# Performance work log

Hardware: AMD Instinct MI355X
Metric: run time of the kernel (lower is better)

The kernel has to match this reference:

```python
import jax, jax.numpy as jnp
import numpy as np

B, NV, H, D = 8, 16, 192, 512
NH = 8
HD = D // NH
DFF = 2048
EPS = 1e-5


def _bn(x, g, b):
    # x: (N, T, C); BatchNorm1d over channel C using batch stats (train mode)
    mu = jnp.mean(x, axis=(0, 1))
    var = jnp.var(x, axis=(0, 1))
    return (x - mu) / jnp.sqrt(var + EPS) * g + b


def _ff(x, w1, b1, w2, b2):
    h = jax.nn.gelu(jnp.einsum('bnhd,fd->bnhf', x, w1) + b1, approximate=False)
    return jnp.einsum('bnhf,df->bnhd', h, w2) + b2


def setup_inputs() -> dict:
    key = jax.random.key(0)
    ks = jax.random.split(key, 20)
    s = 0.02
    return {
        'src': jax.random.normal(ks[0], (B, NV, H, D), jnp.float32),
        'qk_w': jax.random.normal(ks[1], (2 * D, D), jnp.float32) * s,
        'qk_b': jnp.zeros((2 * D,), jnp.float32),
        'v_w': jax.random.normal(ks[2], (D, D), jnp.float32) * s,
        'v_b': jnp.zeros((D,), jnp.float32),
        'alpha_p': jax.random.normal(ks[3], (HD, 1), jnp.float32) * 0.1,
        'g_pre1': jnp.ones((D,), jnp.float32),
        'b_pre1': jnp.zeros((D,), jnp.float32),
        'g_pre2': jnp.ones((D,), jnp.float32),
        'b_pre2': jnp.zeros((D,), jnp.float32),
        'ff1_w1': jax.random.normal(ks[4], (DFF, D), jnp.float32) * s,
        'ff1_b1': jnp.zeros((DFF,), jnp.float32),
        'ff1_w2': jax.random.normal(ks[5], (D, DFF), jnp.float32) * s,
        'ff1_b2': jnp.zeros((D,), jnp.float32),
        'ff2_w1': jax.random.normal(ks[6], (DFF, D), jnp.float32) * s,
        'ff2_b1': jnp.zeros((DFF,), jnp.float32),
        'ff2_w2': jax.random.normal(ks[7], (D, DFF), jnp.float32) * s,
        'ff2_b2': jnp.zeros((D,), jnp.float32),
        'g_attn': jnp.ones((D,), jnp.float32),
        'b_attn': jnp.zeros((D,), jnp.float32),
    }


def reference(src, qk_w, qk_b, v_w, v_b, alpha_p,
              g_pre1, b_pre1, g_pre2, b_pre2,
              ff1_w1, ff1_b1, ff1_w2, ff1_b2,
              ff2_w1, ff2_b1, ff2_w2, ff2_b2,
              g_attn, b_attn):
    b, n, h, c = src.shape
    hd = c // NH
    # normalized input for q,k; raw for v
    src1 = src / jnp.linalg.norm(src, axis=-1, keepdims=True)
    qk = (jnp.einsum('bnhc,ec->bnhe', src1, qk_w) + qk_b)
    qk = qk.reshape(b, n, h, 2, NH, hd).transpose(3, 0, 1, 4, 2, 5)  # (2,b,n,NH,h,hd)
    q, k = qk[0], qk[1]
    v = (jnp.einsum('bnhc,ec->bnhe', src, v_w) + v_b)
    v = v.reshape(b, n, h, NH, hd).transpose(0, 1, 3, 2, 4)  # (b,n,NH,h,hd)

    # exponential-decay weights in FFT domain (branch: h != 7)
    a = jax.nn.sigmoid(alpha_p)                  # (hd,1)
    ar = jnp.arange(h - 1, -1, -1, dtype=src.dtype)
    weights = a * (1.0 - a) ** ar                # (hd, h)
    n2 = 2 * h
    w_f = jnp.fft.rfft(weights, n=n2, axis=-1)   # (hd, h+1)
    q_f = jnp.swapaxes(jnp.fft.rfft(q, n=n2, axis=-2), -1, -2) * w_f
    k_f = jnp.swapaxes(jnp.fft.rfft(k, n=n2, axis=-2), -1, -2) * w_f
    q1 = jnp.swapaxes(jnp.fft.irfft(q_f, n=n2, axis=-1)[..., :h], -1, -2)
    k1 = jnp.swapaxes(jnp.fft.irfft(k_f, n=n2, axis=-1)[..., :h], -1, -2)

    # token-axis attention (note: original divides by head_dim**-0.5 == * sqrt(hd))
    score_t = jnp.einsum('bnhed,bnhfd->bnhef', q1, k1) * (hd ** 0.5)
    attn_t = jax.nn.softmax(score_t, axis=-1)
    out_tok = jnp.einsum('bnhef,bnhfd->bnhed', attn_t, v)  # (b,n,NH,h,hd)
    o3 = _bn(out_tok.reshape(b * n, h, NH * hd), g_pre2, b_pre2).reshape(b, n, h, c)

    # hidden-axis attention on un-decayed q,k (scale = sqrt(h))
    score_h = jnp.einsum('bnhae,bnhaf->bnhef', q, k) * (h ** 0.5)
    attn_h = jax.nn.softmax(score_h, axis=-1)
    out_hid = jnp.einsum('bnhef,bnhaf->bnhae', attn_h, v)  # (b,n,NH,h,hd)
    o2 = _bn(out_hid.reshape(b * n, h, NH * hd), g_pre1, b_pre1).reshape(b, n, h, c)

    src2 = _ff(o3, ff1_w1, ff1_b1, ff1_w2, ff1_b2) + _ff(o2, ff2_w1, ff2_b1, ff2_w2, ff2_b2)
    out = src + src2
    out = _bn(out.reshape(b * n, h, c), g_attn, b_attn).reshape(b, n, h, c)
    return out
```

## Files before the change

### kernel.cpp

```cpp
#include <hip/hip_runtime.h>
#include <math.h>

#define SEQ 192
#define NTOK 24576
#define EPS 1e-5f

typedef __bf16 bf16x8 __attribute__((ext_vector_type(8)));
typedef __bf16 bf16x4 __attribute__((ext_vector_type(4)));
typedef float  f32x4  __attribute__((ext_vector_type(4)));

__device__ __forceinline__ void load_lds16(const __bf16* g, __bf16* l) {
    __builtin_amdgcn_global_load_lds(
        (const __attribute__((address_space(1))) uint32_t*)g,
        (__attribute__((address_space(3))) uint32_t*)l, 16, 0, 0);
}

__device__ __forceinline__ float gelu_f(float x) {
    float z = 1.5957691216057308f * x * fmaf(0.044715f, x*x, 1.f);
    float e = __expf(-z);
    return x * __builtin_amdgcn_rcpf(1.f + e);
}

__global__ __launch_bounds__(256) void cvtall_k(
    const float* __restrict__ s0, const float* __restrict__ s1, const float* __restrict__ s2,
    const float* __restrict__ s3, const float* __restrict__ s4, const float* __restrict__ s5,
    __bf16* __restrict__ dst)
{
    int i = blockIdx.x * 256 + threadIdx.x;
    int f = i * 4;
    const float* s; int off;
    if      (f <  524288) { s = s0; off = 0;       }
    else if (f <  786432) { s = s1; off = 524288;  }
    else if (f < 1835008) { s = s2; off = 786432;  }
    else if (f < 2883584) { s = s3; off = 1835008; }
    else if (f < 3932160) { s = s4; off = 2883584; }
    else                  { s = s5; off = 3932160; }
    f32x4 v = *(const f32x4*)&s[f - off];
    bf16x4 o;
    o[0]=(__bf16)v[0]; o[1]=(__bf16)v[1]; o[2]=(__bf16)v[2]; o[3]=(__bf16)v[3];
    ((bf16x4*)dst)[i] = o;
}

__global__ __launch_bounds__(256) void prep_k(const float* __restrict__ src,
    __bf16* __restrict__ srcb, __bf16* __restrict__ srcnb)
{
    int w = threadIdx.x >> 6, lane = threadIdx.x & 63;
    size_t token = blockIdx.x * 4 + w;
    const float* p = src + token * 512 + lane * 8;
    f32x4 a0 = *(const f32x4*)p;
    f32x4 a1 = *(const f32x4*)(p + 4);
    float s = a0[0]*a0[0]+a0[1]*a0[1]+a0[2]*a0[2]+a0[3]*a0[3]
            + a1[0]*a1[0]+a1[1]*a1[1]+a1[2]*a1[2]+a1[3]*a1[3];
#pragma unroll
    for (int off = 32; off; off >>= 1) s += __shfl_xor(s, off);
    float rs = rsqrtf(s);
    bf16x8 vb, vn;
#pragma unroll
    for (int q = 0; q < 4; q++) {
        vb[q]   = (__bf16)a0[q];      vn[q]   = (__bf16)(a0[q]*rs);
        vb[q+4] = (__bf16)a1[q];      vn[q+4] = (__bf16)(a1[q]*rs);
    }
    *(bf16x8*)&srcb[token*512 + lane*8]  = vb;
    *(bf16x8*)&srcnb[token*512 + lane*8] = vn;
}

template<bool AFFINE, bool GELU>
__global__ __launch_bounds__(256) void gemm_k(
    const __bf16* __restrict__ A, const __bf16* __restrict__ B, __bf16* __restrict__ C,
    int N, int K, const float* __restrict__ bias, const float* __restrict__ coef)
{
    __shared__ __bf16 As[8192];
    __shared__ __bf16 Bs[8192];
    const int tid = threadIdx.x, lane = tid & 63, w = tid >> 6;
    const int wr = w >> 1, wc = w & 1;
    const int b = blockIdx.y * gridDim.x + blockIdx.x;
    const int xcd = b & 7, bi = b >> 3;
    const int ypx = gridDim.y >> 3;
    const int m0 = (xcd * ypx + bi / gridDim.x) * 128;
    const int n0 = (bi % gridDim.x) * 128;
    const int fr = lane & 15, fq = lane >> 4;
    const int grow = 8*w + (lane >> 3);
    const int gcol = ((lane & 7) ^ (lane >> 3)) * 8;
    const __bf16* gB = B + (size_t)(n0 + grow) * K + gcol;
    const __bf16* gA = A + (size_t)(m0 + grow) * K + gcol;
    __bf16* ldsA = As + 8*w*64 + lane*8;
    __bf16* ldsB = Bs + 8*w*64 + lane*8;

    f32x4 acc[4][4];
#pragma unroll
    for (int i = 0; i < 4; i++)
#pragma unroll
        for (int j = 0; j < 4; j++) acc[i][j] = (f32x4){0.f,0.f,0.f,0.f};

    for (int k0 = 0; k0 < K; k0 += 64) {
        if (!AFFINE) {
#pragma unroll
            for (int i = 0; i < 4; i++)
                load_lds16(gA + k0 + (size_t)(32*i)*K, ldsA + i*2048);
        } else {
            const int r = tid >> 3, cseg = tid & 7;
            const float* scp = coef + k0 + cseg*8;
            const float* shp = coef + 512 + k0 + cseg*8;
            f32x4 sc0 = *(const f32x4*)scp, sc1 = *(const f32x4*)(scp+4);
            f32x4 sh0 = *(const f32x4*)shp, sh1 = *(const f32x4*)(shp+4);
#pragma unroll
            for (int i = 0; i < 4; i++) {
                int row = 32*i + r;
                bf16x8 a = *(const bf16x8*)&A[(size_t)(m0+row)*512 + k0 + cseg*8];
                bf16x8 v;
#pragma unroll
                for (int q = 0; q < 4; q++) {
                    v[q]   = (__bf16)fmaf((float)a[q],   sc0[q], sh0[q]);
                    v[q+4] = (__bf16)fmaf((float)a[q+4], sc1[q], sh1[q]);
                }
                *(bf16x8*)&As[row*64 + ((cseg ^ (r & 7)) * 8)] = v;
            }
        }
#pragma unroll
        for (int i = 0; i < 4; i++)
            load_lds16(gB + k0 + (size_t)(32*i)*K, ldsB + i*2048);
        __syncthreads();
#pragma unroll
        for (int kk = 0; kk < 2; kk++) {
            bf16x8 af[4], bfv[4];
#pragma unroll
            for (int i = 0; i < 4; i++)
                af[i] = *(bf16x8*)&As[(wr*64 + i*16 + fr)*64 + (((kk*4+fq) ^ (fr&7))*8)];
#pragma unroll
            for (int j = 0; j < 4; j++)
                bfv[j] = *(bf16x8*)&Bs[(wc*64 + j*16 + fr)*64 + (((kk*4+fq) ^ (fr&7))*8)];
#pragma unroll
            for (int i = 0; i < 4; i++)
#pragma unroll
                for (int j = 0; j < 4; j++)
                    acc[i][j] = __builtin_amdgcn_mfma_f32_16x16x32_bf16(af[i], bfv[j], acc[i][j], 0, 0, 0);
        }
        __syncthreads();
    }
    const int r4 = lane >> 4, cc = lane & 15;
#pragma unroll
    for (int i = 0; i < 4; i++) {
#pragma unroll
        for (int r = 0; r < 4; r++) {
            int m = m0 + wr*64 + i*16 + r4*4 + r;
#pragma unroll
            for (int j = 0; j < 4; j++) {
                int n = n0 + wc*64 + j*16 + cc;
                float v = acc[i][j][r] + bias[n];
                if (GELU) v = gelu_f(v);
                C[(size_t)m * N + n] = (__bf16)v;
            }
        }
    }
}

__global__ __launch_bounds__(256) void gemm2_k(
    const __bf16* __restrict__ A1, const __bf16* __restrict__ A2,
    const __bf16* __restrict__ B1, const __bf16* __restrict__ B2,
    float* __restrict__ C, const float* __restrict__ b1, const float* __restrict__ b2,
    const float* __restrict__ resid, float* __restrict__ st)
{
    __shared__ __bf16 As[4096];
    __shared__ __bf16 Bs[8192];
    const int tid = threadIdx.x, lane = tid & 63, w = tid >> 6;
    const int wr = w >> 1, wc = w & 1;
    const int vb = blockIdx.x;
    const int xcd = vb & 7, k2 = vb >> 3;
    const int m0 = (xcd*24 + (k2 >> 2)) * 64;
    const int n0 = (k2 & 3) * 128;
    const int fr = lane & 15, fq = lane >> 4;
    const int grow = 8*w + (lane >> 3);
    const int gcol = ((lane & 7) ^ (lane >> 3)) * 8;
    const int K = 2048;
    __bf16* ldsA = As + 8*w*64 + lane*8;
    __bf16* ldsB = Bs + 8*w*64 + lane*8;

    f32x4 acc[2][4];
#pragma unroll
    for (int i = 0; i < 2; i++)
#pragma unroll
        for (int j = 0; j < 4; j++) acc[i][j] = (f32x4){0.f,0.f,0.f,0.f};

#pragma unroll 1
    for (int half = 0; half < 2; half++) {
        const __bf16* gA = (half ? A2 : A1) + (size_t)(m0 + grow) * K + gcol;
        const __bf16* gB = (half ? B2 : B1) + (size_t)(n0 + grow) * K + gcol;
        for (int k0 = 0; k0 < K; k0 += 64) {
            load_lds16(gA + k0,                 ldsA);
            load_lds16(gA + k0 + (size_t)32*K,  ldsA + 2048);
#pragma unroll
            for (int i = 0; i < 4; i++)
                load_lds16(gB + k0 + (size_t)(32*i)*K, ldsB + i*2048);
            __syncthreads();
#pragma unroll
            for (int kk = 0; kk < 2; kk++) {
                bf16x8 af[2], bfv[4];
#pragma unroll
                for (int i = 0; i < 2; i++)
                    af[i] = *(bf16x8*)&As[(wr*32 + i*16 + fr)*64 + (((kk*4+fq) ^ (fr&7))*8)];
#pragma unroll
                for (int j = 0; j < 4; j++)
                    bfv[j] = *(bf16x8*)&Bs[(wc*64 + j*16 + fr)*64 + (((kk*4+fq) ^ (fr&7))*8)];
#pragma unroll
                for (int i = 0; i < 2; i++)
#pragma unroll
                    for (int j = 0; j < 4; j++)
                        acc[i][j] = __builtin_amdgcn_mfma_f32_16x16x32_bf16(af[i], bfv[j], acc[i][j], 0, 0, 0);
            }
            __syncthreads();
        }
    }
    const int r4 = lane >> 4, cc = lane & 15;
    float cs[4] = {0,0,0,0}, cq[4] = {0,0,0,0};
#pragma unroll
    for (int i = 0; i < 2; i++) {
#pragma unroll
        for (int r = 0; r < 4; r++) {
            int m = m0 + wr*32 + i*16 + r4*4 + r;
#pragma unroll
            for (int j = 0; j < 4; j++) {
                int n = n0 + wc*64 + j*16 + cc;
                size_t idx = (size_t)m * 512 + n;
                float v = acc[i][j][r] + b1[n] + b2[n] + resid[idx];
                C[idx] = v;
                cs[j] += v; cq[j] = fmaf(v, v, cq[j]);
            }
        }
    }
#pragma unroll
    for (int j = 0; j < 4; j++) {
        cs[j] += __shfl_xor(cs[j], 16); cs[j] += __shfl_xor(cs[j], 32);
        cq[j] += __shfl_xor(cq[j], 16); cq[j] += __shfl_xor(cq[j], 32);
    }
    if (r4 == 0) {
#pragma unroll
        for (int j = 0; j < 4; j++) {
            int n = n0 + wc*64 + j*16 + cc;
            atomicAdd(&st[n], cs[j]);
            atomicAdd(&st[512 + n], cq[j]);
        }
    }
}

__global__ __launch_bounds__(256) void decay_scan_k(__bf16* __restrict__ QKb, const float* __restrict__ alpha)
{
    int g = blockIdx.x * 256 + threadIdx.x;
    int bn = g >> 8, e4 = (g & 255) * 4;
    int ai = e4 & 63;
    f32x4 a, rr;
#pragma unroll
    for (int j = 0; j < 4; j++) { float av = 1.f/(1.f + __expf(-alpha[ai + j])); a[j] = av; rr[j] = 1.f - av; }
    __bf16* p = QKb + (size_t)bn * SEQ * 1024 + e4;
    f32x4 P = {0,0,0,0}, pw = {1,1,1,1};
    for (int t = 0; t < SEQ; t++) {
        bf16x4 v = *(bf16x4*)&p[(size_t)t*1024];
        f32x4 vf = { (float)v[0], (float)v[1], (float)v[2], (float)v[3] };
        P += pw * vf;
        bf16x4 o;
#pragma unroll
        for (int j = 0; j < 4; j++) o[j] = (__bf16)P[j];
        *(bf16x4*)&p[(size_t)t*1024] = o;
        pw *= rr;
    }
    f32x4 f = a;
    for (int t = SEQ-1; t >= 0; t--) {
        bf16x4 v = *(bf16x4*)&p[(size_t)t*1024];
        bf16x4 o;
#pragma unroll
        for (int j = 0; j < 4; j++) o[j] = (__bf16)((float)v[j] * f[j]);
        *(bf16x4*)&p[(size_t)t*1024] = o;
        f *= rr;
    }
}

__global__ __launch_bounds__(256) void hidden_attn_mfma_k(
    const __bf16* __restrict__ QKb, const __bf16* __restrict__ Vb, __bf16* __restrict__ OHb)
{
    __shared__ __bf16 smem[25600];
    __bf16* Qt = smem;
    __bf16* Kt = smem + 12800;
    __bf16* Ps = smem;
    __bf16* Vs = smem + 4608;
    const int bn = blockIdx.x >> 3, nh = blockIdx.x & 7;
    const int tid = threadIdx.x, lane = tid & 63, w = tid >> 6;
    const int fr = lane & 15, fq = lane >> 4;
    const size_t rowbase = (size_t)bn * SEQ;

#pragma unroll
    for (int it = 0; it < 12; it++) {
        int tk = tid + (it % 6) * 256;
        int j = tk & 63, tg = tk >> 6;
        const __bf16* gsrc = QKb + (rowbase + tg*8)*1024 + nh*64 + j + (it >= 6 ? 512 : 0);
        bf16x8 v;
#pragma unroll
        for (int u = 0; u < 8; u++) v[u] = gsrc[(size_t)u*1024];
        __bf16* dst = (it >= 6 ? Kt : Qt) + j*200 + tg*8;
        *(bf16x8*)dst = v;
    }
    __syncthreads();

    f32x4 acc[4];
#pragma unroll
    for (int i = 0; i < 4; i++) acc[i] = (f32x4){0.f,0.f,0.f,0.f};
#pragma unroll
    for (int kc = 0; kc < 6; kc++) {
        bf16x8 a = *(bf16x8*)&Qt[(w*16 + fr)*200 + kc*32 + fq*8];
#pragma unroll
        for (int nt = 0; nt < 4; nt++) {
            bf16x8 b = *(bf16x8*)&Kt[(nt*16 + fr)*200 + kc*32 + fq*8];
            acc[nt] = __builtin_amdgcn_mfma_f32_16x16x32_bf16(a, b, acc[nt], 0, 0, 0);
        }
    }
    const float sc = 13.856406460551018f;
    float pn[4][4];
#pragma unroll
    for (int reg = 0; reg < 4; reg++) {
        float m = -1e30f;
#pragma unroll
        for (int nt = 0; nt < 4; nt++) { acc[nt][reg] *= sc; m = fmaxf(m, acc[nt][reg]); }
#pragma unroll
        for (int off = 1; off < 16; off <<= 1) m = fmaxf(m, __shfl_xor(m, off));
        float l = 0.f;
#pragma unroll
        for (int nt = 0; nt < 4; nt++) { pn[nt][reg] = __expf(acc[nt][reg] - m); l += pn[nt][reg]; }
#pragma unroll
        for (int off = 1; off < 16; off <<= 1) l += __shfl_xor(l, off);
        float inv = 1.f / l;
#pragma unroll
        for (int nt = 0; nt < 4; nt++) pn[nt][reg] *= inv;
    }
    __syncthreads();
#pragma unroll
    for (int nt = 0; nt < 4; nt++)
#pragma unroll
        for (int reg = 0; reg < 4; reg++)
            Ps[(w*16 + fq*4 + reg)*72 + nt*16 + fr] = (__bf16)pn[nt][reg];
    for (int i = tid; i < 1536; i += 256) {
        int t = i >> 3, s = i & 7;
        *(bf16x8*)&Vs[t*72 + s*8] = *(const bf16x8*)&Vb[(rowbase+t)*512 + nh*64 + s*8];
    }
    __syncthreads();

    f32x4 o[3][4];
#pragma unroll
    for (int i = 0; i < 3; i++)
#pragma unroll
        for (int j = 0; j < 4; j++) o[i][j] = (f32x4){0.f,0.f,0.f,0.f};
#pragma unroll
    for (int kc = 0; kc < 2; kc++) {
        bf16x8 av[3];
#pragma unroll
        for (int mt = 0; mt < 3; mt++)
            av[mt] = *(bf16x8*)&Vs[(48*w + mt*16 + fr)*72 + kc*32 + fq*8];
#pragma unroll
        for (int nt = 0; nt < 4; nt++) {
            bf16x8 b = *(bf16x8*)&Ps[(nt*16 + fr)*72 + kc*32 + fq*8];
#pragma unroll
            for (int mt = 0; mt < 3; mt++)
                o[mt][nt] = __builtin_amdgcn_mfma_f32_16x16x32_bf16(av[mt], b, o[mt][nt], 0, 0, 0);
        }
    }
    __bf16* obase = OHb + ((size_t)(bn*8 + nh)) * SEQ * 64;
#pragma unroll
    for (int mt = 0; mt < 3; mt++)
#pragma unroll
        for (int reg = 0; reg < 4; reg++) {
            int t = 48*w + mt*16 + fq*4 + reg;
#pragma unroll
            for (int nt = 0; nt < 4; nt++)
                obase[(size_t)t*64 + nt*16 + fr] = (__bf16)o[mt][nt][reg];
        }
}

__global__ __launch_bounds__(256) void token_attn_mfma_k(
    const __bf16* __restrict__ QKb, const __bf16* __restrict__ Vb, __bf16* __restrict__ OT)
{
    __shared__ __bf16 smem[27648];
    __bf16* Qs = smem;
    __bf16* Ks = smem + 13824;
    __bf16* Vt = smem;
    __bf16* Pw = smem + 12800;
    const int bn = blockIdx.x >> 3, nh = blockIdx.x & 7;
    const int tid = threadIdx.x, lane = tid & 63, w = tid >> 6;
    const int fr = lane & 15, fq = lane >> 4;
    const size_t rowbase = (size_t)bn * SEQ;

    for (int i = tid; i < 1536; i += 256) {
        int t = i >> 3, s = i & 7;
        const __bf16* g = QKb + (rowbase + t)*1024 + nh*64;
        *(bf16x8*)&Qs[t*72 + s*8] = *(const bf16x8*)&g[s*8];
        *(bf16x8*)&Ks[t*72 + s*8] = *(const bf16x8*)&g[512 + s*8];
    }
    __syncthreads();

    f32x4 S[3][12];
#pragma unroll
    for (int i = 0; i < 3; i++)
#pragma unroll
        for (int j = 0; j < 12; j++) S[i][j] = (f32x4){0.f,0.f,0.f,0.f};
#pragma unroll
    for (int kc = 0; kc < 2; kc++) {
        bf16x8 aq[3];
#pragma unroll
        for (int mt = 0; mt < 3; mt++)
            aq[mt] = *(bf16x8*)&Qs[(48*w + mt*16 + fr)*72 + kc*32 + fq*8];
#pragma unroll
        for (int nt = 0; nt < 12; nt++) {
            bf16x8 b = *(bf16x8*)&Ks[(nt*16 + fr)*72 + kc*32 + fq*8];
#pragma unroll
            for (int mt = 0; mt < 3; mt++)
                S[mt][nt] = __builtin_amdgcn_mfma_f32_16x16x32_bf16(aq[mt], b, S[mt][nt], 0, 0, 0);
        }
    }
#pragma unroll
    for (int mt = 0; mt < 3; mt++)
#pragma unroll
        for (int reg = 0; reg < 4; reg++) {
            float m = -1e30f;
#pragma unroll
            for (int nt = 0; nt < 12; nt++) { S[mt][nt][reg] *= 8.f; m = fmaxf(m, S[mt][nt][reg]); }
#pragma unroll
            for (int off = 1; off < 16; off <<= 1) m = fmaxf(m, __shfl_xor(m, off));
            float l = 0.f;
#pragma unroll
            for (int nt = 0; nt < 12; nt++) { S[mt][nt][reg] = __expf(S[mt][nt][reg] - m); l += S[mt][nt][reg]; }
#pragma unroll
            for (int off = 1; off < 16; off <<= 1) l += __shfl_xor(l, off);
            float inv = 1.f / l;
#pragma unroll
            for (int nt = 0; nt < 12; nt++) S[mt][nt][reg] *= inv;
        }
    __syncthreads();
#pragma unroll
    for (int it = 0; it < 6; it++) {
        int tk = tid + it * 256;
        int d = tk & 63, tg = tk >> 6;
        const __bf16* gsrc = Vb + (rowbase + tg*8)*512 + nh*64 + d;
        bf16x8 v;
#pragma unroll
        for (int u = 0; u < 8; u++) v[u] = gsrc[(size_t)u*512];
        *(bf16x8*)&Vt[d*200 + tg*8] = v;
    }
    __syncthreads();

    f32x4 O[3][4];
#pragma unroll
    for (int i = 0; i < 3; i++)
#pragma unroll
        for (int j = 0; j < 4; j++) O[i][j] = (f32x4){0.f,0.f,0.f,0.f};
    __bf16* myP = Pw + w*3456;
#pragma unroll
    for (int fc = 0; fc < 3; fc++) {
#pragma unroll
        for (int mt = 0; mt < 3; mt++)
#pragma unroll
            for (int j = 0; j < 4; j++)
#pragma unroll
                for (int reg = 0; reg < 4; reg++)
                    myP[(mt*16 + fq*4 + reg)*72 + j*16 + fr] = (__bf16)S[mt][fc*4 + j][reg];
#pragma unroll
        for (int kc = 0; kc < 2; kc++) {
            bf16x8 ap[3];
#pragma unroll
            for (int mt = 0; mt < 3; mt++)
                ap[mt] = *(bf16x8*)&myP[(mt*16 + fr)*72 + kc*32 + fq*8];
#pragma unroll
            for (int dt = 0; dt < 4; dt++) {
                bf16x8 b = *(bf16x8*)&Vt[(dt*16 + fr)*200 + fc*64 + kc*32 + fq*8];
#pragma unroll
                for (int mt = 0; mt < 3; mt++)
                    O[mt][dt] = __builtin_amdgcn_mfma_f32_16x16x32_bf16(ap[mt], b, O[mt][dt], 0, 0, 0);
            }
        }
    }
    __bf16* obase = OT + ((size_t)(bn*8 + nh)) * SEQ * 64;
#pragma unroll
    for (int mt = 0; mt < 3; mt++)
#pragma unroll
        for (int reg = 0; reg < 4; reg++) {
            int e = 48*w + mt*16 + fq*4 + reg;
#pragma unroll
            for (int dt = 0; dt < 4; dt++)
                obase[(size_t)e*64 + dt*16 + fr] = (__bf16)O[mt][dt][reg];
        }
}

__global__ __launch_bounds__(256) void bn_stats1_k(const __bf16* __restrict__ x, float* __restrict__ part)
{
    __shared__ float red[3072];
    const int col8 = threadIdx.x & 63;
    const int rl   = threadIdx.x >> 6;
    const size_t r0 = (size_t)blockIdx.x * 96;
    f32x4 sA = {0,0,0,0}, sB = {0,0,0,0}, qA = {0,0,0,0}, qB = {0,0,0,0};
    for (int r = rl; r < 96; r += 4) {
        bf16x8 v = *(const bf16x8*)&x[(r0 + r)*512 + col8*8];
        f32x4 lo = { (float)v[0], (float)v[1], (float)v[2], (float)v[3] };
        f32x4 hi = { (float)v[4], (float)v[5], (float)v[6], (float)v[7] };
        sA += lo; sB += hi;
        qA += lo*lo; qB += hi*hi;
    }
    if (rl > 0) {
        float* p = &red[(rl-1)*1024];
        *(f32x4*)&p[col8*8]       = sA;  *(f32x4*)&p[col8*8 + 4]       = sB;
        *(f32x4*)&p[512 + col8*8] = qA;  *(f32x4*)&p[512 + col8*8 + 4] = qB;
    }
    __syncthreads();
    if (rl == 0) {
#pragma unroll
        for (int k = 0; k < 3; k++) {
            float* p = &red[k*1024];
            sA += *(f32x4*)&p[col8*8];       sB += *(f32x4*)&p[col8*8 + 4];
            qA += *(f32x4*)&p[512 + col8*8]; qB += *(f32x4*)&p[512 + col8*8 + 4];
        }
        float* o = &part[(size_t)blockIdx.x * 1024];
        *(f32x4*)&o[col8*8]       = sA;  *(f32x4*)&o[col8*8 + 4]       = sB;
        *(f32x4*)&o[512 + col8*8] = qA;  *(f32x4*)&o[512 + col8*8 + 4] = qB;
    }
}

__global__ __launch_bounds__(256) void bn_stats2_k(const float* __restrict__ part, float* __restrict__ st)
{
    int c = blockIdx.x * 256 + threadIdx.x;
    float s0 = 0.f, s1 = 0.f, s2 = 0.f, s3 = 0.f;
    for (int b = 0; b < 256; b += 4) {
        s0 += part[(size_t)b*1024 + c];
        s1 += part[(size_t)(b+1)*1024 + c];
        s2 += part[(size_t)(b+2)*1024 + c];
        s3 += part[(size_t)(b+3)*1024 + c];
    }
    st[c] = (s0 + s1) + (s2 + s3);
}

__global__ void bn_coef_k(const float* __restrict__ st, const float* __restrict__ g,
                          const float* __restrict__ b, float* __restrict__ coef)
{
    int c = threadIdx.x;
    float mean = st[c] * (1.f/24576.f);
    float var  = st[512+c] * (1.f/24576.f) - mean*mean;
    float sc = rsqrtf(var + EPS) * g[c];
    coef[c] = sc;
    coef[512 + c] = b[c] - mean * sc;
}

__global__ __launch_bounds__(256) void bn_apply4_k(const float* __restrict__ x, const float* __restrict__ st,
    const float* __restrict__ g, const float* __restrict__ b, float* __restrict__ out)
{
    size_t i = (size_t)blockIdx.x * 256 + threadIdx.x;
    int col4 = i & 127;
    f32x4 v = ((const f32x4*)x)[i];
    f32x4 sm = ((const f32x4*)st)[col4];
    f32x4 sq = ((const f32x4*)(st + 512))[col4];
    f32x4 o;
#pragma unroll
    for (int j = 0; j < 4; j++) {
        int c = col4*4 + j;
        float mean = sm[j] * (1.f/24576.f);
        float var  = sq[j] * (1.f/24576.f) - mean*mean;
        o[j] = (v[j] - mean) * rsqrtf(var + EPS) * g[c] + b[c];
    }
    ((f32x4*)out)[i] = o;
}

extern "C" void kernel_launch(void* const* d_in, const int* in_sizes, int n_in,
                              void* d_out, int out_size, void* d_ws, size_t ws_size,
                              hipStream_t stream)
{
    const float* src    = (const float*)d_in[0];
    const float* qk_w   = (const float*)d_in[1];
    const float* qk_b   = (const float*)d_in[2];
    const float* v_w    = (const float*)d_in[3];
    const float* v_b    = (const float*)d_in[4];
    const float* alpha  = (const float*)d_in[5];
    const float* g_pre1 = (const float*)d_in[6];
    const float* b_pre1 = (const float*)d_in[7];
    const float* g_pre2 = (const float*)d_in[8];
    const float* b_pre2 = (const float*)d_in[9];
    const float* ff1_w1 = (const float*)d_in[10];
    const float* ff1_b1 = (const float*)d_in[11];
    const float* ff1_w2 = (const float*)d_in[12];
    const float* ff1_b2 = (const float*)d_in[13];
    const float* ff2_w1 = (const float*)d_in[14];
    const float* ff2_b1 = (const float*)d_in[15];
    const float* ff2_w2 = (const float*)d_in[16];
    const float* ff2_b2 = (const float*)d_in[17];
    const float* g_attn = (const float*)d_in[18];
    const float* b_attn = (const float*)d_in[19];
    float* out = (float*)d_out;

    __bf16* wq   = (__bf16*)d_ws;
    __bf16* wv   = wq  + 524288;
    __bf16* w11  = wv  + 262144;
    __bf16* w12  = w11 + 1048576;
    __bf16* w21  = w12 + 1048576;
    __bf16* w22  = w21 + 1048576;
    __bf16* srcb  = w22 + 1048576;
    __bf16* srcnb = srcb + (size_t)NTOK*512;
    __bf16* QKb   = srcnb + (size_t)NTOK*512;
    __bf16* Vb    = QKb + (size_t)NTOK*1024;
    __bf16* OHbf  = Vb + (size_t)NTOK*512;
    __bf16* o3bf  = OHbf + (size_t)NTOK*512;
    float*  stats = (float*)(o3bf + (size_t)NTOK*512);
    float*  coef0 = stats + 3072;
    float*  coef1 = coef0 + 1024;
    float*  part0 = coef1 + 1024;
    float*  part1 = part0 + 262144;
    __bf16* H1 = srcb;
    __bf16* H2 = H1 + (size_t)12288*2048;
    float *st0 = stats, *st1 = stats + 1024, *st2 = stats + 2048;

    hipMemsetAsync(st2, 0, 1024*sizeof(float), stream);

    cvtall_k<<<4864, 256, 0, stream>>>(qk_w, v_w, ff1_w1, ff1_w2, ff2_w1, ff2_w2, wq);
    prep_k<<<NTOK/4, 256, 0, stream>>>(src, srcb, srcnb);

    gemm_k<false,false><<<dim3(8, 192), 256, 0, stream>>>(srcnb, wq, QKb, 1024, 512, qk_b, nullptr);
    gemm_k<false,false><<<dim3(4, 192), 256, 0, stream>>>(srcb,  wv, Vb,  512,  512, v_b,  nullptr);

    hidden_attn_mfma_k<<<1024, 256, 0, stream>>>(QKb, Vb, OHbf);

    decay_scan_k<<<128, 256, 0, stream>>>(QKb, alpha);
    token_attn_mfma_k<<<1024, 256, 0, stream>>>(QKb, Vb, o3bf);

    bn_stats1_k<<<256, 256, 0, stream>>>(o3bf, part0);
    bn_stats1_k<<<256, 256, 0, stream>>>(OHbf, part1);
    bn_stats2_k<<<4, 256, 0, stream>>>(part0, st0);
    bn_stats2_k<<<4, 256, 0, stream>>>(part1, st1);
    bn_coef_k<<<1, 512, 0, stream>>>(st0, g_pre2, b_pre2, coef0);
    bn_coef_k<<<1, 512, 0, stream>>>(st1, g_pre1, b_pre1, coef1);

    for (int ch = 0; ch < 2; ch++) {
        size_t off = (size_t)ch * 12288 * 512;
        gemm_k<true,true><<<dim3(16, 96), 256, 0, stream>>>(o3bf + off, w11, H1, 2048, 512, ff1_b1, coef0);
        gemm_k<true,true><<<dim3(16, 96), 256, 0, stream>>>(OHbf + off, w21, H2, 2048, 512, ff2_b1, coef1);
        gemm2_k<<<768, 256, 0, stream>>>(H1, H2, w12, w22, out + off,
                                         ff1_b2, ff2_b2, src + off, st2);
    }

    bn_apply4_k<<<12288, 256, 0, stream>>>(out, st2, g_attn, b_attn, out);
}
```

Before: 705.1 us.

## Fuse decay scan into token attention and fold BN affine into FF1 weights

Removes the standalone decay_scan kernel, which makes two strided global passes over Q/K. The scan now runs inside token_attn on the LDS tiles, with one thread per column doing sequential prefix and suffix passes. Separately, the pre-FF BatchNorm scale and shift are folded into the first FF weight matrix and bias by a small w1scale kernel, so the FF1 GEMM no longer applies the per-element normalization on its A operand. Risks include serial scan latency inside the attention block, LDS bank conflicts from the 72-element stride, and bf16 rounding of the rescaled weights.

Measured after the change: 696.9 us. About the same (-1.2%).

```diff
diff --git a/kernel.cpp b/kernel.cpp
--- a/kernel.cpp
+++ b/kernel.cpp
@@ -154,6 +154,34 @@
     }
 }
 
+__global__ __launch_bounds__(256) void w1scale_k(
+    __bf16* __restrict__ w, const float* __restrict__ coef,
+    const float* __restrict__ bias_in, float* __restrict__ bias_out)
+{
+    const int wv = threadIdx.x >> 6, lane = threadIdx.x & 63;
+    const int n = blockIdx.x * 4 + wv;
+    __bf16* p = w + (size_t)n * 512 + lane * 8;
+    bf16x8 v = *(bf16x8*)p;
+    f32x4 sc0 = *(const f32x4*)(coef + lane*8);
+    f32x4 sc1 = *(const f32x4*)(coef + lane*8 + 4);
+    f32x4 sh0 = *(const f32x4*)(coef + 512 + lane*8);
+    f32x4 sh1 = *(const f32x4*)(coef + 512 + lane*8 + 4);
+    float dot = 0.f;
+    bf16x8 o;
+#pragma unroll
+    for (int q = 0; q < 4; q++) {
+        float w0 = (float)v[q], w1 = (float)v[q+4];
+        o[q]   = (__bf16)(w0 * sc0[q]);
+        o[q+4] = (__bf16)(w1 * sc1[q]);
+        dot = fmaf(w0, sh0[q], dot);
+        dot = fmaf(w1, sh1[q], dot);
+    }
+    *(bf16x8*)p = o;
+#pragma unroll
+    for (int off = 32; off; off >>= 1) dot += __shfl_xor(dot, off);
+    if (lane == 0) bias_out[n] = bias_in[n] + dot;
+}
+
 __global__ __launch_bounds__(256) void gemm2_k(
     const __bf16* __restrict__ A1, const __bf16* __restrict__ A2,
     const __bf16* __restrict__ B1, const __bf16* __restrict__ B2,
@@ -242,37 +270,6 @@
     }
 }
 
-__global__ __launch_bounds__(256) void decay_scan_k(__bf16* __restrict__ QKb, const float* __restrict__ alpha)
-{
-    int g = blockIdx.x * 256 + threadIdx.x;
-    int bn = g >> 8, e4 = (g & 255) * 4;
-    int ai = e4 & 63;
-    f32x4 a, rr;
-#pragma unroll
-    for (int j = 0; j < 4; j++) { float av = 1.f/(1.f + __expf(-alpha[ai + j])); a[j] = av; rr[j] = 1.f - av; }
-    __bf16* p = QKb + (size_t)bn * SEQ * 1024 + e4;
-    f32x4 P = {0,0,0,0}, pw = {1,1,1,1};
-    for (int t = 0; t < SEQ; t++) {
-        bf16x4 v = *(bf16x4*)&p[(size_t)t*1024];
-        f32x4 vf = { (float)v[0], (float)v[1], (float)v[2], (float)v[3] };
-        P += pw * vf;
-        bf16x4 o;
-#pragma unroll
-        for (int j = 0; j < 4; j++) o[j] = (__bf16)P[j];
-        *(bf16x4*)&p[(size_t)t*1024] = o;
-        pw *= rr;
-    }
-    f32x4 f = a;
-    for (int t = SEQ-1; t >= 0; t--) {
-        bf16x4 v = *(bf16x4*)&p[(size_t)t*1024];
-        bf16x4 o;
-#pragma unroll
-        for (int j = 0; j < 4; j++) o[j] = (__bf16)((float)v[j] * f[j]);
-        *(bf16x4*)&p[(size_t)t*1024] = o;
-        f *= rr;
-    }
-}
-
 __global__ __launch_bounds__(256) void hidden_attn_mfma_k(
     const __bf16* __restrict__ QKb, const __bf16* __restrict__ Vb, __bf16* __restrict__ OHb)
 {
@@ -373,7 +370,8 @@
 }
 
 __global__ __launch_bounds__(256) void token_attn_mfma_k(
-    const __bf16* __restrict__ QKb, const __bf16* __restrict__ Vb, __bf16* __restrict__ OT)
+    const __bf16* __restrict__ QKb, const __bf16* __restrict__ Vb, __bf16* __restrict__ OT,
+    const float* __restrict__ alpha)
 {
     __shared__ __bf16 smem[27648];
     __bf16* Qs = smem;
@@ -390,6 +388,27 @@
         const __bf16* g = QKb + (rowbase + t)*1024 + nh*64;
         *(bf16x8*)&Qs[t*72 + s*8] = *(const bf16x8*)&g[s*8];
         *(bf16x8*)&Ks[t*72 + s*8] = *(const bf16x8*)&g[512 + s*8];
+    }
+    __syncthreads();
+
+    if (tid < 128) {
+        const int d = tid & 63;
+        __bf16* col = (tid < 64) ? (Qs + d) : (Ks + d);
+        const float av = 1.f / (1.f + __expf(-alpha[d]));
+        const float r = 1.f - av;
+        float P = 0.f, pw = 1.f;
+#pragma unroll 4
+        for (int t = 0; t < SEQ; t++) {
+            P = fmaf(pw, (float)col[t*72], P);
+            col[t*72] = (__bf16)P;
+            pw *= r;
+        }
+        float f = av;
+#pragma unroll 4
+        for (int t = SEQ-1; t >= 0; t--) {
+            col[t*72] = (__bf16)((float)col[t*72] * f);
+            f *= r;
+        }
     }
     __syncthreads();
 
@@ -604,6 +623,8 @@
     float*  coef1 = coef0 + 1024;
     float*  part0 = coef1 + 1024;
     float*  part1 = part0 + 262144;
+    float*  bias1p = part1 + 262144;
+    float*  bias2p = bias1p + 2048;
     __bf16* H1 = srcb;
     __bf16* H2 = H1 + (size_t)12288*2048;
     float *st0 = stats, *st1 = stats + 1024, *st2 = stats + 2048;
@@ -618,8 +639,7 @@
 
     hidden_attn_mfma_k<<<1024, 256, 0, stream>>>(QKb, Vb, OHbf);
 
-    decay_scan_k<<<128, 256, 0, stream>>>(QKb, alpha);
-    token_attn_mfma_k<<<1024, 256, 0, stream>>>(QKb, Vb, o3bf);
+    token_attn_mfma_k<<<1024, 256, 0, stream>>>(QKb, Vb, o3bf, alpha);
 
     bn_stats1_k<<<256, 256, 0, stream>>>(o3bf, part0);
     bn_stats1_k<<<256, 256, 0, stream>>>(OHbf, part1);
@@ -627,11 +647,13 @@
     bn_stats2_k<<<4, 256, 0, stream>>>(part1, st1);
     bn_coef_k<<<1, 512, 0, stream>>>(st0, g_pre2, b_pre2, coef0);
     bn_coef_k<<<1, 512, 0, stream>>>(st1, g_pre1, b_pre1, coef1);
+    w1scale_k<<<512, 256, 0, stream>>>(w11, coef0, ff1_b1, bias1p);
+    w1scale_k<<<512, 256, 0, stream>>>(w21, coef1, ff2_b1, bias2p);
 
     for (int ch = 0; ch < 2; ch++) {
         size_t off = (size_t)ch * 12288 * 512;
-        gemm_k<true,true><<<dim3(16, 96), 256, 0, stream>>>(o3bf + off, w11, H1, 2048, 512, ff1_b1, coef0);
-        gemm_k<true,true><<<dim3(16, 96), 256, 0, stream>>>(OHbf + off, w21, H2, 2048, 512, ff2_b1, coef1);
+        gemm_k<false,true><<<dim3(16, 96), 256, 0, stream>>>(o3bf + off, w11, H1, 2048, 512, bias1p, nullptr);
+        gemm_k<false,true><<<dim3(16, 96), 256, 0, stream>>>(OHbf + off, w21, H2, 2048, 512, bias2p, nullptr);
         gemm2_k<<<768, 256, 0, stream>>>(H1, H2, w12, w22, out + off,
                                          ff1_b2, ff2_b2, src + off, st2);
     }
```
